# Optimization experiments

Hardware: AMD Instinct MI355X
Metric: run time of the kernel (lower is better)

## Reference

```python
import jax, jax.numpy as jnp
import numpy as np

T = 512   # timesteps (also used as batch-index count for packing)
B = 512   # batch (must equal T for this module's packing to be consistent)
D = 300   # state_dim
H = 128   # hidden_state_dim
E = 64    # embedding_dim
EGO = 12  # ego_state slice fed to the LSTMCell


def setup_inputs() -> dict:
    key = jax.random.key(0)
    ks = jax.random.split(key, 10)
    k = float(1.0 / np.sqrt(H))  # torch LSTMCell uniform init bound
    state = jax.random.normal(ks[0], (T, B, D), dtype=jnp.float32)
    hidden_state = jax.random.normal(ks[1], (B, H), dtype=jnp.float32) * 0.1
    cell_state = jax.random.normal(ks[2], (B, H), dtype=jnp.float32) * 0.1
    len_sequence = jax.random.randint(ks[3], (T,), 1, T + 1, dtype=jnp.int64 if jax.config.jax_enable_x64 else jnp.int32)
    W_ih = jax.random.uniform(ks[4], (4 * H, EGO), minval=-k, maxval=k, dtype=jnp.float32)
    W_hh = jax.random.uniform(ks[5], (4 * H, H), minval=-k, maxval=k, dtype=jnp.float32)
    b_ih = jax.random.uniform(ks[6], (4 * H,), minval=-k, maxval=k, dtype=jnp.float32)
    b_hh = jax.random.uniform(ks[7], (4 * H,), minval=-k, maxval=k, dtype=jnp.float32)
    W_emb = jax.random.normal(ks[8], (E, D + H), dtype=jnp.float32) * 0.05
    b_emb = jnp.zeros((E,), dtype=jnp.float32)
    return dict(state=state, hidden_state=hidden_state, cell_state=cell_state,
                len_sequence=len_sequence, W_ih=W_ih, W_hh=W_hh, b_ih=b_ih,
                b_hh=b_hh, W_emb=W_emb, b_emb=b_emb)


def _pack_indices(L):
    # tmp_output[t][:L[t]] concat over t -> flat indices into [T*B, .] (row-major t,b)
    idx_rnn = np.concatenate([t * B + np.arange(int(L[t])) for t in range(T)]) if T else np.zeros((0,), np.int32)
    # state.permute(1,0,2)[b][:L[b]] concat over b -> flat indices into [B*T, .] (row-major b,t)
    idx_state = np.concatenate([b * T + np.arange(int(L[b])) for b in range(B)]) if B else np.zeros((0,), np.int32)
    return jnp.asarray(idx_rnn, jnp.int32), jnp.asarray(idx_state, jnp.int32)


def _lstm_scan(x_seq, h0, c0, W_ih, W_hh, b_ih, b_hh):
    # torch.nn.LSTMCell math; gate order [i, f, g, o]
    def step(carry, x_t):
        h, c = carry
        gates = x_t @ W_ih.T + b_ih + h @ W_hh.T + b_hh  # [B, 4H]
        i, f, g, o = jnp.split(gates, 4, axis=-1)
        c_new = jax.nn.sigmoid(f) * c + jax.nn.sigmoid(i) * jnp.tanh(g)
        h_new = jax.nn.sigmoid(o) * jnp.tanh(c_new)
        return (h_new, c_new), h_new
    _, hs = jax.lax.scan(step, (h0, c0), x_seq)
    return hs  # [T, B, H]


def reference(state, hidden_state, cell_state, len_sequence, W_ih, W_hh, b_ih, b_hh, W_emb, b_emb):
    L = np.asarray(len_sequence)
    idx_rnn, idx_state = _pack_indices(L)
    rnn_input = state[:, :, :EGO]                               # [T, B, 12]
    hs = _lstm_scan(rnn_input, hidden_state, cell_state, W_ih, W_hh, b_ih, b_hh)  # [T, B, H]
    rnn_packed = hs.reshape(T * B, H)[idx_rnn]                  # [N, H]
    state_packed = jnp.transpose(state, (1, 0, 2)).reshape(B * T, D)[idx_state]  # [N, D]
    feats = jnp.concatenate([state_packed, rnn_packed], axis=1)  # [N, D+H]
    return feats @ W_emb.T + b_emb                               # [N, E]
```

## Files before the change

### kernel.cpp

```cpp
#include <hip/hip_runtime.h>
#include <hip/hip_fp16.h>

#define T_ 512
#define B_ 512
#define D_ 300
#define H_ 128
#define E_ 64
#define EGO_ 12
#define DH_ 428
#define BD_ 153600

typedef __attribute__((ext_vector_type(2))) _Float16 half2_t;
typedef __attribute__((ext_vector_type(8))) _Float16 half8_t;
typedef __attribute__((ext_vector_type(4))) float float4_t;

__device__ __forceinline__ unsigned pack2(float a, float b) {
  __half2 h = __floats2half2_rn(a, b);
  return __builtin_bit_cast(unsigned, h);
}
__device__ __forceinline__ half8_t h8(uint4 u) {
  return __builtin_bit_cast(half8_t, u);
}
__device__ __forceinline__ float sigm(float x) {
  float e = __builtin_amdgcn_exp2f(-1.4426950408889634f * x);
  return __builtin_amdgcn_rcpf(1.0f + e);
}
__device__ __forceinline__ float tanh_(float x) {
  float e = __builtin_amdgcn_exp2f(2.8853900817779268f * x);
  return 1.0f - 2.0f * __builtin_amdgcn_rcpf(1.0f + e);
}

__global__ void prefix_k(const int* __restrict__ L, int* __restrict__ pfx) {
  __shared__ int s[T_];
  int t = threadIdx.x;
  s[t] = L[t];
  __syncthreads();
  for (int off = 1; off < T_; off <<= 1) {
    int v = 0;
    if (t >= off) v = s[t - off];
    __syncthreads();
    s[t] += v;
    __syncthreads();
  }
  if (t == 0) pfx[0] = 0;
  pfx[t + 1] = s[t];
}

#define WS_ 84
__launch_bounds__(256, 1)
__global__ void scan_k(const float* __restrict__ state,
                       const float* __restrict__ h0,
                       const float* __restrict__ c0,
                       const int* __restrict__ lens,
                       const float* __restrict__ W_ih,
                       const float* __restrict__ W_hh,
                       const float* __restrict__ b_ih,
                       const float* __restrict__ b_hh,
                       const float* __restrict__ W_emb,
                       const float* __restrict__ b_emb,
                       const int* __restrict__ pfx,
                       float* __restrict__ out) {
  __shared__ __align__(16) unsigned hb[2][16][WS_];
  __shared__ int pfx_s[T_], len_s[T_];

  const int tid  = threadIdx.x;
  const int lane = tid & 63;
  const int w    = tid >> 6;
  const int n16  = lane & 15;
  const int quad = lane >> 4;
  const int b0   = blockIdx.x * 2;

  uint4 bfr[4][2][5];
  float bias[4][2];
#pragma unroll
  for (int c = 0; c < 4; ++c) {
#pragma unroll
    for (int p = 0; p < 2; ++p) {
      const int g = c * 128 + w * 32 + 2 * n16 + p;
      bias[c][p] = b_ih[g] + b_hh[g];
#pragma unroll
      for (int s = 0; s < 5; ++s) {
        unsigned pk[4];
#pragma unroll
        for (int pp = 0; pp < 4; ++pp) {
          const int k0 = s * 32 + quad * 8 + 2 * pp;
          float f0 = 0.f, f1 = 0.f;
          if (k0 < 128) { f0 = W_hh[g * H_ + k0]; f1 = W_hh[g * H_ + k0 + 1]; }
          else if (k0 < 140) {
            f0 = W_ih[g * EGO_ + (k0 - 128)];
            if (k0 + 1 < 140) f1 = W_ih[g * EGO_ + (k0 - 127)];
          }
          pk[pp] = pack2(f0, f1);
        }
        bfr[c][p][s] = make_uint4(pk[0], pk[1], pk[2], pk[3]);
      }
    }
  }
  uint4 efr[4];
  const int e_ = w * 16 + n16;
  const float bemb = b_emb[e_];
#pragma unroll
  for (int s = 0; s < 4; ++s) {
    unsigned pk[4];
#pragma unroll
    for (int pp = 0; pp < 4; ++pp) {
      const int k0 = s * 32 + quad * 8 + 2 * pp;
      pk[pp] = pack2(W_emb[e_ * DH_ + D_ + k0], W_emb[e_ * DH_ + D_ + k0 + 1]);
    }
    efr[s] = make_uint4(pk[0], pk[1], pk[2], pk[3]);
  }

  for (int i = tid; i < 2 * 16 * WS_; i += 256) ((unsigned*)hb)[i] = 0u;
  for (int i = tid; i < T_; i += 256) { pfx_s[i] = pfx[i]; len_s[i] = lens[i]; }
  __syncthreads();
  if (tid < 128) {
    const int r = tid >> 6, d = tid & 63;
    float2 v = ((const float2*)(h0 + (b0 + r) * H_))[d];
    hb[0][r][d] = pack2(v.x, v.y);
  }
  float2 xheld = make_float2(0.f, 0.f);
  if (tid >= 16 && tid < 28) {
    const int j = tid - 16, row = j / 6, jj = j % 6;
    float2 v = ((const float2*)(state + (b0 + row) * D_))[jj];
    hb[0][row][64 + jj] = pack2(v.x, v.y);
    xheld = ((const float2*)(state + BD_ + (b0 + row) * D_))[jj];
  }
  float cst[2][2] = {{0.f, 0.f}, {0.f, 0.f}};
  if (quad == 0) {
#pragma unroll
    for (int r = 0; r < 2; ++r)
#pragma unroll
      for (int p = 0; p < 2; ++p)
        cst[r][p] = c0[(b0 + r) * H_ + w * 32 + 2 * n16 + p];
  }
  __syncthreads();

#pragma unroll 1
  for (int t = 0; t < T_; ++t) {
    const int pb = t & 1;
    float2 xnew = xheld;
    if (tid >= 16 && tid < 28) {
      const int j = tid - 16, row = j / 6, jj = j % 6;
      const int ttx = (t + 2 < T_) ? t + 2 : T_ - 1;
      xnew = ((const float2*)(state + (size_t)ttx * BD_ + (b0 + row) * D_))[jj];
    }

    uint4 a[5];
#pragma unroll
    for (int s = 0; s < 5; ++s)
      a[s] = *(const uint4*)(&hb[pb][n16][s * 16 + quad * 4]);

    if (t > 0) {
      float4_t ea = (float4_t){0.f, 0.f, 0.f, 0.f};
#pragma unroll
      for (int s = 0; s < 4; ++s)
        ea = __builtin_amdgcn_mfma_f32_16x16x32_f16(h8(a[s]), h8(efr[s]), ea, 0, 0, 0);
      if (quad == 0) {
        const int Lt = len_s[t - 1];
        const size_t base = (size_t)pfx_s[t - 1] + b0;
        if (b0 < Lt)     out[base * E_ + e_]       = ea[0] + bemb;
        if (b0 + 1 < Lt) out[(base + 1) * E_ + e_] = ea[1] + bemb;
      }
    }

    float4_t acc[4][2];
#pragma unroll
    for (int c = 0; c < 4; ++c)
#pragma unroll
      for (int p = 0; p < 2; ++p) acc[c][p] = (float4_t){0.f, 0.f, 0.f, 0.f};
#pragma unroll
    for (int s = 0; s < 5; ++s) {
      const half8_t ah = h8(a[s]);
#pragma unroll
      for (int c = 0; c < 4; ++c)
#pragma unroll
        for (int p = 0; p < 2; ++p)
          acc[c][p] = __builtin_amdgcn_mfma_f32_16x16x32_f16(ah, h8(bfr[c][p][s]), acc[c][p], 0, 0, 0);
    }

    if (quad == 0) {
#pragma unroll
      for (int r = 0; r < 2; ++r) {
        float hp[2];
#pragma unroll
        for (int p = 0; p < 2; ++p) {
          const float gi = acc[0][p][r] + bias[0][p];
          const float gf = acc[1][p][r] + bias[1][p];
          const float gg = acc[2][p][r] + bias[2][p];
          const float go = acc[3][p][r] + bias[3][p];
          const float cc = sigm(gf) * cst[r][p] + sigm(gi) * tanh_(gg);
          cst[r][p] = cc;
          hp[p] = sigm(go) * tanh_(cc);
        }
        hb[1 - pb][r][w * 16 + n16] = pack2(hp[0], hp[1]);
      }
    }
    if (tid >= 16 && tid < 28) {
      const int j = tid - 16, row = j / 6, jj = j % 6;
      hb[1 - pb][row][64 + jj] = pack2(xheld.x, xheld.y);
      xheld = xnew;
    }
    __syncthreads();
  }

  {
    float4_t ea = (float4_t){0.f, 0.f, 0.f, 0.f};
#pragma unroll
    for (int s = 0; s < 4; ++s) {
      uint4 a = *(const uint4*)(&hb[0][n16][s * 16 + quad * 4]);
      ea = __builtin_amdgcn_mfma_f32_16x16x32_f16(h8(a), h8(efr[s]), ea, 0, 0, 0);
    }
    if (quad == 0) {
      const int Lt = len_s[T_ - 1];
      const size_t base = (size_t)pfx_s[T_ - 1] + b0;
      if (b0 < Lt)     out[base * E_ + e_]       = ea[0] + bemb;
      if (b0 + 1 < Lt) out[(base + 1) * E_ + e_] = ea[1] + bemb;
    }
  }
}

#define ER_ 16
#define ES_ 164
__launch_bounds__(256, 4)
__global__ void emb_state_k(const float* __restrict__ state,
                            const float* __restrict__ W_emb,
                            const int* __restrict__ pfx,
                            float* __restrict__ out, int N) {
  __shared__ __align__(16) unsigned srow[ER_][ES_];
  __shared__ int rk[ER_], rj[ER_];

  const int tid  = threadIdx.x;
  const int lane = tid & 63;
  const int w    = tid >> 6;
  const int n16  = lane & 15;
  const int quad = lane >> 4;
  const int r0   = blockIdx.x * ER_;

  uint4 efr[10];
  const int e_ = w * 16 + n16;
#pragma unroll
  for (int s = 0; s < 10; ++s) {
    unsigned pk[4];
#pragma unroll
    for (int pp = 0; pp < 4; ++pp) {
      const int k0 = s * 32 + quad * 8 + 2 * pp;
      float f0 = 0.f, f1 = 0.f;
      if (k0 < D_) {
        f0 = W_emb[e_ * DH_ + k0];
        if (k0 + 1 < D_) f1 = W_emb[e_ * DH_ + k0 + 1];
      }
      pk[pp] = pack2(f0, f1);
    }
    efr[s] = make_uint4(pk[0], pk[1], pk[2], pk[3]);
  }

  if (tid < ER_) {
    int r = r0 + tid;
    int k = -1, j = 0;
    if (r < N) {
      int lo = 0, hi = T_;
      while (hi - lo > 1) {
        int mid = (lo + hi) >> 1;
        if (pfx[mid] <= r) lo = mid; else hi = mid;
      }
      k = lo; j = r - pfx[lo];
    }
    rk[tid] = k; rj[tid] = j;
  }
  __syncthreads();

  {
    const int row = tid >> 4, i = tid & 15;
    const int k = rk[row];
    const float4* sp = (const float4*)(state + ((size_t)rj[row] * B_ + (k < 0 ? 0 : k)) * D_);
#pragma unroll 1
    for (int c4 = i; c4 < 82; c4 += 16) {
      unsigned p0 = 0u, p1 = 0u;
      if (k >= 0 && c4 < 75) {
        float4 f = sp[c4];
        p0 = pack2(f.x, f.y); p1 = pack2(f.z, f.w);
      }
      srow[row][2 * c4] = p0;
      srow[row][2 * c4 + 1] = p1;
    }
  }
  __syncthreads();

  float4_t acc = (float4_t){0.f, 0.f, 0.f, 0.f};
#pragma unroll
  for (int s = 0; s < 10; ++s) {
    uint4 a = *(const uint4*)(&srow[n16][s * 16 + quad * 4]);
    acc = __builtin_amdgcn_mfma_f32_16x16x32_f16(h8(a), h8(efr[s]), acc, 0, 0, 0);
  }
#pragma unroll
  for (int r = 0; r < 4; ++r) {
    const int R = r0 + quad * 4 + r;
    if (R < N) out[(size_t)R * E_ + e_] += acc[r];
  }
}

extern "C" void kernel_launch(void* const* d_in, const int* in_sizes, int n_in,
                              void* d_out, int out_size, void* d_ws, size_t ws_size,
                              hipStream_t stream) {
  const float* state = (const float*)d_in[0];
  const float* h0    = (const float*)d_in[1];
  const float* c0    = (const float*)d_in[2];
  const int*   lens  = (const int*)d_in[3];
  const float* W_ih  = (const float*)d_in[4];
  const float* W_hh  = (const float*)d_in[5];
  const float* b_ih  = (const float*)d_in[6];
  const float* b_hh  = (const float*)d_in[7];
  const float* W_emb = (const float*)d_in[8];
  const float* b_emb = (const float*)d_in[9];
  float* out = (float*)d_out;
  int* pfx = (int*)d_ws;
  const int N = out_size / E_;

  prefix_k<<<1, T_, 0, stream>>>(lens, pfx);
  scan_k<<<B_ / 2, 256, 0, stream>>>(state, h0, c0, lens, W_ih, W_hh, b_ih, b_hh,
                                     W_emb, b_emb, pfx, out);
  emb_state_k<<<(N + ER_ - 1) / ER_, 256, 0, stream>>>(state, W_emb, pfx, out, N);
}
```

Baseline: 917.0 us.

## Spread LSTM rows across quads, fold biases into MFMA init, persist embedding kernel

```diff
diff --git a/kernel.cpp b/kernel.cpp
--- a/kernel.cpp
+++ b/kernel.cpp
@@ -116,22 +116,20 @@
   if (tid < 128) {
     const int r = tid >> 6, d = tid & 63;
     float2 v = ((const float2*)(h0 + (b0 + r) * H_))[d];
-    hb[0][r][d] = pack2(v.x, v.y);
+    hb[0][4 * r][d] = pack2(v.x, v.y);
   }
   float2 xheld = make_float2(0.f, 0.f);
   if (tid >= 16 && tid < 28) {
     const int j = tid - 16, row = j / 6, jj = j % 6;
     float2 v = ((const float2*)(state + (b0 + row) * D_))[jj];
-    hb[0][row][64 + jj] = pack2(v.x, v.y);
+    hb[0][4 * row][64 + jj] = pack2(v.x, v.y);
     xheld = ((const float2*)(state + BD_ + (b0 + row) * D_))[jj];
   }
-  float cst[2][2] = {{0.f, 0.f}, {0.f, 0.f}};
-  if (quad == 0) {
-#pragma unroll
-    for (int r = 0; r < 2; ++r)
-#pragma unroll
-      for (int p = 0; p < 2; ++p)
-        cst[r][p] = c0[(b0 + r) * H_ + w * 32 + 2 * n16 + p];
+  float cst[2] = {0.f, 0.f};
+  if (quad < 2) {
+#pragma unroll
+    for (int p = 0; p < 2; ++p)
+      cst[p] = c0[(b0 + quad) * H_ + w * 32 + 2 * n16 + p];
   }
   __syncthreads();
 
@@ -151,15 +149,14 @@
       a[s] = *(const uint4*)(&hb[pb][n16][s * 16 + quad * 4]);
 
     if (t > 0) {
-      float4_t ea = (float4_t){0.f, 0.f, 0.f, 0.f};
+      float4_t ea = (float4_t){bemb, bemb, bemb, bemb};
 #pragma unroll
       for (int s = 0; s < 4; ++s)
         ea = __builtin_amdgcn_mfma_f32_16x16x32_f16(h8(a[s]), h8(efr[s]), ea, 0, 0, 0);
-      if (quad == 0) {
+      if (quad < 2) {
         const int Lt = len_s[t - 1];
-        const size_t base = (size_t)pfx_s[t - 1] + b0;
-        if (b0 < Lt)     out[base * E_ + e_]       = ea[0] + bemb;
-        if (b0 + 1 < Lt) out[(base + 1) * E_ + e_] = ea[1] + bemb;
+        if (b0 + quad < Lt)
+          out[((size_t)pfx_s[t - 1] + b0 + quad) * E_ + e_] = ea[0];
       }
     }
 
@@ -167,7 +164,8 @@
 #pragma unroll
     for (int c = 0; c < 4; ++c)
 #pragma unroll
-      for (int p = 0; p < 2; ++p) acc[c][p] = (float4_t){0.f, 0.f, 0.f, 0.f};
+      for (int p = 0; p < 2; ++p)
+        acc[c][p] = (float4_t){bias[c][p], bias[c][p], bias[c][p], bias[c][p]};
 #pragma unroll
     for (int s = 0; s < 5; ++s) {
       const half8_t ah = h8(a[s]);
@@ -178,63 +176,58 @@
           acc[c][p] = __builtin_amdgcn_mfma_f32_16x16x32_f16(ah, h8(bfr[c][p][s]), acc[c][p], 0, 0, 0);
     }
 
-    if (quad == 0) {
-#pragma unroll
-      for (int r = 0; r < 2; ++r) {
-        float hp[2];
-#pragma unroll
-        for (int p = 0; p < 2; ++p) {
-          const float gi = acc[0][p][r] + bias[0][p];
-          const float gf = acc[1][p][r] + bias[1][p];
-          const float gg = acc[2][p][r] + bias[2][p];
-          const float go = acc[3][p][r] + bias[3][p];
-          const float cc = sigm(gf) * cst[r][p] + sigm(gi) * tanh_(gg);
-          cst[r][p] = cc;
-          hp[p] = sigm(go) * tanh_(cc);
-        }
-        hb[1 - pb][r][w * 16 + n16] = pack2(hp[0], hp[1]);
+    if (quad < 2) {
+      float hp[2];
+#pragma unroll
+      for (int p = 0; p < 2; ++p) {
+        const float gi = acc[0][p][0];
+        const float gf = acc[1][p][0];
+        const float gg = acc[2][p][0];
+        const float go = acc[3][p][0];
+        const float cc = sigm(gf) * cst[p] + sigm(gi) * tanh_(gg);
+        cst[p] = cc;
+        hp[p] = sigm(go) * tanh_(cc);
       }
+      hb[1 - pb][quad * 4][w * 16 + n16] = pack2(hp[0], hp[1]);
     }
     if (tid >= 16 && tid < 28) {
       const int j = tid - 16, row = j / 6, jj = j % 6;
-      hb[1 - pb][row][64 + jj] = pack2(xheld.x, xheld.y);
+      hb[1 - pb][4 * row][64 + jj] = pack2(xheld.x, xheld.y);
       xheld = xnew;
     }
     __syncthreads();
   }
 
   {
-    float4_t ea = (float4_t){0.f, 0.f, 0.f, 0.f};
+    float4_t ea = (float4_t){bemb, bemb, bemb, bemb};
 #pragma unroll
     for (int s = 0; s < 4; ++s) {
       uint4 a = *(const uint4*)(&hb[0][n16][s * 16 + quad * 4]);
       ea = __builtin_amdgcn_mfma_f32_16x16x32_f16(h8(a), h8(efr[s]), ea, 0, 0, 0);
     }
-    if (quad == 0) {
+    if (quad < 2) {
       const int Lt = len_s[T_ - 1];
-      const size_t base = (size_t)pfx_s[T_ - 1] + b0;
-      if (b0 < Lt)     out[base * E_ + e_]       = ea[0] + bemb;
-      if (b0 + 1 < Lt) out[(base + 1) * E_ + e_] = ea[1] + bemb;
+      if (b0 + quad < Lt)
+        out[((size_t)pfx_s[T_ - 1] + b0 + quad) * E_ + e_] = ea[0];
     }
   }
 }
 
 #define ER_ 16
-#define ES_ 164
-__launch_bounds__(256, 4)
+__launch_bounds__(256, 3)
 __global__ void emb_state_k(const float* __restrict__ state,
                             const float* __restrict__ W_emb,
                             const int* __restrict__ pfx,
                             float* __restrict__ out, int N) {
-  __shared__ __align__(16) unsigned srow[ER_][ES_];
-  __shared__ int rk[ER_], rj[ER_];
+  __shared__ int pfx_s[T_ + 1];
 
   const int tid  = threadIdx.x;
   const int lane = tid & 63;
   const int w    = tid >> 6;
   const int n16  = lane & 15;
   const int quad = lane >> 4;
-  const int r0   = blockIdx.x * ER_;
+
+  for (int i = tid; i <= T_; i += 256) pfx_s[i] = pfx[i];
 
   uint4 efr[10];
   const int e_ = w * 16 + n16;
@@ -253,49 +246,48 @@
     }
     efr[s] = make_uint4(pk[0], pk[1], pk[2], pk[3]);
   }
-
-  if (tid < ER_) {
-    int r = r0 + tid;
-    int k = -1, j = 0;
-    if (r < N) {
-      int lo = 0, hi = T_;
-      while (hi - lo > 1) {
-        int mid = (lo + hi) >> 1;
-        if (pfx[mid] <= r) lo = mid; else hi = mid;
-      }
-      k = lo; j = r - pfx[lo];
-    }
-    rk[tid] = k; rj[tid] = j;
-  }
   __syncthreads();
 
-  {
-    const int row = tid >> 4, i = tid & 15;
-    const int k = rk[row];
-    const float4* sp = (const float4*)(state + ((size_t)rj[row] * B_ + (k < 0 ? 0 : k)) * D_);
-#pragma unroll 1
-    for (int c4 = i; c4 < 82; c4 += 16) {
-      unsigned p0 = 0u, p1 = 0u;
-      if (k >= 0 && c4 < 75) {
-        float4 f = sp[c4];
-        p0 = pack2(f.x, f.y); p1 = pack2(f.z, f.w);
-      }
-      srow[row][2 * c4] = p0;
-      srow[row][2 * c4 + 1] = p1;
-    }
-  }
-  __syncthreads();
-
-  float4_t acc = (float4_t){0.f, 0.f, 0.f, 0.f};
-#pragma unroll
-  for (int s = 0; s < 10; ++s) {
-    uint4 a = *(const uint4*)(&srow[n16][s * 16 + quad * 4]);
-    acc = __builtin_amdgcn_mfma_f32_16x16x32_f16(h8(a), h8(efr[s]), acc, 0, 0, 0);
-  }
-#pragma unroll
-  for (int r = 0; r < 4; ++r) {
-    const int R = r0 + quad * 4 + r;
-    if (R < N) out[(size_t)R * E_ + e_] += acc[r];
+  const int ntiles = (N + ER_ - 1) / ER_;
+  for (int tile = blockIdx.x; tile < ntiles; tile += gridDim.x) {
+    const int r0 = tile * ER_;
+    int rA = r0 + n16;
+    if (rA > N - 1) rA = N - 1;
+    int lo = 0, hi = T_;
+#pragma unroll
+    for (int it = 0; it < 9; ++it) {
+      const int mid = (lo + hi) >> 1;
+      if (pfx_s[mid] <= rA) lo = mid; else hi = mid;
+    }
+    const float4* sp4 =
+        (const float4*)(state + ((size_t)(rA - pfx_s[lo]) * B_ + lo) * D_) + quad * 2;
+
+    float4 a0[10], a1[10];
+#pragma unroll
+    for (int s = 0; s < 9; ++s) { a0[s] = sp4[8 * s]; a1[s] = sp4[8 * s + 1]; }
+    {
+      const float4 z = make_float4(0.f, 0.f, 0.f, 0.f);
+      a0[9] = (quad < 2) ? sp4[72] : z;
+      a1[9] = (quad == 0) ? sp4[73] : z;
+    }
+
+    float4_t acc0 = (float4_t){0.f, 0.f, 0.f, 0.f};
+    float4_t acc1 = (float4_t){0.f, 0.f, 0.f, 0.f};
+#pragma unroll
+    for (int s = 0; s < 10; ++s) {
+      uint4 ua;
+      ua.x = pack2(a0[s].x, a0[s].y);
+      ua.y = pack2(a0[s].z, a0[s].w);
+      ua.z = pack2(a1[s].x, a1[s].y);
+      ua.w = pack2(a1[s].z, a1[s].w);
+      if (s & 1) acc1 = __builtin_amdgcn_mfma_f32_16x16x32_f16(h8(ua), h8(efr[s]), acc1, 0, 0, 0);
+      else       acc0 = __builtin_amdgcn_mfma_f32_16x16x32_f16(h8(ua), h8(efr[s]), acc0, 0, 0, 0);
+    }
+#pragma unroll
+    for (int r = 0; r < 4; ++r) {
+      const int R = r0 + quad * 4 + r;
+      if (R < N) out[(size_t)R * E_ + e_] += acc0[r] + acc1[r];
+    }
   }
 }
 
@@ -319,5 +311,7 @@
   prefix_k<<<1, T_, 0, stream>>>(lens, pfx);
   scan_k<<<B_ / 2, 256, 0, stream>>>(state, h0, c0, lens, W_ih, W_hh, b_ih, b_hh,
                                      W_emb, b_emb, pfx, out);
-  emb_state_k<<<(N + ER_ - 1) / ER_, 256, 0, stream>>>(state, W_emb, pfx, out, N);
-}
+  const int ntiles = (N + ER_ - 1) / ER_;
+  const int g = ntiles < 768 ? ntiles : 768;
+  emb_state_k<<<g, 256, 0, stream>>>(state, W_emb, pfx, out, N);
+}
```

Result: faster. 835.2 us (-8.9%).
